# Kernel optimization log

Hardware: AMD Instinct MI355X
Metric: run time of the kernel (lower is better)

The kernel has to match this reference:

```python
import jax, jax.numpy as jnp
import numpy as np

H = 8        # num_heads
D = 64       # qkv_dim
E = 512      # embed_dim = H*D
MS = 16      # ms_hidden_dim


def setup_inputs() -> dict:
    key = jax.random.key(0)
    ks = jax.random.split(key, 12)
    b, r, c = 4, 512, 512
    row_emb = jax.random.normal(ks[0], (b, r, E), dtype=jnp.float32)
    col_emb = jax.random.normal(ks[1], (b, c, E), dtype=jnp.float32)
    cost_mat = jax.random.uniform(ks[2], (b, r, c), dtype=jnp.float32)
    attn_mask = jax.random.randint(ks[3], (b, H, r, c), 0, 2) > 0
    s = 1.0 / np.sqrt(E)
    Wq = jax.random.uniform(ks[4], (H * D, E), minval=-s, maxval=s)
    Wk = jax.random.uniform(ks[5], (H * D, E), minval=-s, maxval=s)
    Wv = jax.random.uniform(ks[6], (H * D, E), minval=-s, maxval=s)
    Wout = jax.random.uniform(ks[7], (E, E), minval=-s, maxval=s)
    m1 = np.sqrt(0.5)
    m2 = np.sqrt(1.0 / MS)
    Wmix1 = jax.random.uniform(ks[8], (H * MS, 2 * H), minval=-m1, maxval=m1)
    Wmix2 = jax.random.uniform(ks[9], (H, H * MS), minval=-m2, maxval=m2)
    return {"row_emb": row_emb, "col_emb": col_emb, "cost_mat": cost_mat,
            "attn_mask": attn_mask, "Wq": Wq, "Wk": Wk, "Wv": Wv,
            "Wmix1": Wmix1, "Wmix2": Wmix2, "Wout": Wout}


def reference(row_emb, col_emb, cost_mat, attn_mask, Wq, Wk, Wv, Wmix1, Wmix2, Wout):
    b, r, _ = row_emb.shape
    c = col_emb.shape[1]
    norm = 1.0 / jnp.sqrt(jnp.asarray(D, row_emb.dtype))
    # projections -> [b, h, s, d]
    q = (row_emb @ Wq.T).reshape(b, r, H, D).transpose(0, 2, 1, 3)
    k = (col_emb @ Wk.T).reshape(b, c, H, D).transpose(0, 2, 1, 3)
    v = (col_emb @ Wv.T).reshape(b, c, H, D).transpose(0, 2, 1, 3)
    dot = norm * jnp.einsum('bhrd,bhcd->bhrc', q, k)            # [b,h,r,c]
    cost = jnp.broadcast_to(cost_mat[:, None, :, :], dot.shape)  # [b,h,r,c]
    # stack then rearrange 'b h r c s -> b r c (h s)' (h major, s minor)
    two = jnp.stack([dot, cost], axis=-1)                        # [b,h,r,c,2]
    two = two.transpose(0, 2, 3, 1, 4).reshape(b, r, c, 2 * H)
    hid = jax.nn.relu(two @ Wmix1.T)                             # [b,r,c,H*MS]
    ms = hid @ Wmix2.T                                           # [b,r,c,H]
    logits = ms.transpose(0, 3, 1, 2)                            # [b,h,r,c]
    # mask handling: rows that are fully masked become fully unmasked
    all_masked = jnp.all(attn_mask, axis=-1, keepdims=True)
    mask = jnp.where(all_masked, False, attn_mask)
    logits = jnp.where(mask, -jnp.inf, logits)
    weights = jax.nn.softmax(logits, axis=-1)
    out = jnp.einsum('bhrc,bhcd->bhrd', weights, v)              # [b,h,r,d]
    out = out.transpose(0, 2, 1, 3).reshape(b, r, H * D)         # b s (h d)
    return out @ Wout.T
```

## Files before the change

### kernel.cpp

```cpp
#include <hip/hip_runtime.h>
#include <math.h>

typedef __attribute__((ext_vector_type(8))) short bf16x8;
typedef __attribute__((ext_vector_type(4))) float f32x4;
typedef unsigned short ushort_t;

static __device__ inline unsigned short f2bf(float f) {
    union { float f; unsigned u; } v; v.f = f;
    unsigned r = v.u + 0x7fff + ((v.u >> 16) & 1);
    return (unsigned short)(r >> 16);
}

#if defined(__has_builtin)
#  if __has_builtin(__builtin_amdgcn_cvt_pk_bf16_f32)
#    define HAVE_PK_BF16 1
#  endif
#endif

static __device__ inline unsigned pk2bf(float a, float b) {
#ifdef HAVE_PK_BF16
    auto r = __builtin_amdgcn_cvt_pk_bf16_f32(a, b);
    unsigned u; __builtin_memcpy(&u, &r, 4);
    return u;
#else
    return (unsigned)f2bf(a) | ((unsigned)f2bf(b) << 16);
#endif
}

__global__ __launch_bounds__(256) void convert_all(const float* __restrict__ a0,
                                                   const float* __restrict__ a1,
                                                   const float* __restrict__ a2,
                                                   const float* __restrict__ a3,
                                                   const float* __restrict__ a4,
                                                   const float* __restrict__ a5,
                                                   ushort_t* __restrict__ dst) {
    const size_t e = ((size_t)blockIdx.x * 256 + threadIdx.x) * 4;
    const float* src; size_t off;
    if      (e < 1048576) { src = a0; off = 0; }
    else if (e < 2097152) { src = a1; off = 1048576; }
    else if (e < 2359296) { src = a2; off = 2097152; }
    else if (e < 2621440) { src = a3; off = 2359296; }
    else if (e < 2883584) { src = a4; off = 2621440; }
    else                  { src = a5; off = 2883584; }
    const float4 v = *(const float4*)(src + (e - off));
    uint2 o; o.x = pk2bf(v.x, v.y); o.y = pk2bf(v.z, v.w);
    *(uint2*)(dst + e) = o;
}

__global__ __launch_bounds__(256) void gemm_qkv(const ushort_t* __restrict__ rowb,
                                                const ushort_t* __restrict__ colb,
                                                const ushort_t* __restrict__ Wqb,
                                                const ushort_t* __restrict__ Wkb,
                                                const ushort_t* __restrict__ Wvb,
                                                ushort_t* __restrict__ Qb,
                                                ushort_t* __restrict__ Kb,
                                                ushort_t* __restrict__ Vt) {
    const int z = blockIdx.z;
    const ushort_t* A = (z == 0) ? rowb : colb;
    const ushort_t* B = (z == 0) ? Wqb : (z == 1) ? Wkb : Wvb;

    const int t    = threadIdx.x;
    const int w    = t >> 6;
    const int lane = t & 63;
    const int quad = lane >> 4;
    const int sl   = lane & 15;
    const int m0 = blockIdx.x * 64 + (w >> 1) * 32;
    const int n0 = blockIdx.y * 64 + (w & 1) * 32;

    f32x4 acc[2][2] = {};

    for (int k0 = 0; k0 < 512; k0 += 32) {
        bf16x8 a[2], b[2];
#pragma unroll
        for (int rs = 0; rs < 2; ++rs)
            a[rs] = *(const bf16x8*)(A + (size_t)(m0 + rs * 16 + sl) * 512 + k0 + quad * 8);
#pragma unroll
        for (int cs = 0; cs < 2; ++cs)
            b[cs] = *(const bf16x8*)(B + (size_t)(n0 + cs * 16 + sl) * 512 + k0 + quad * 8);
#pragma unroll
        for (int rs = 0; rs < 2; ++rs)
#pragma unroll
            for (int cs = 0; cs < 2; ++cs)
                acc[rs][cs] = __builtin_amdgcn_mfma_f32_16x16x32_bf16(a[rs], b[cs], acc[rs][cs], 0, 0, 0);
    }

#pragma unroll
    for (int rs = 0; rs < 2; ++rs)
#pragma unroll
        for (int cs = 0; cs < 2; ++cs) {
            const int n = n0 + cs * 16 + sl;
            if (z == 2) {
                const int mb   = m0 + rs * 16 + quad * 4;
                const int bidx = mb >> 9, c = mb & 511;
                const int h = n >> 6, d = n & 63;
                ushort4 o;
                o.x = f2bf(acc[rs][cs][0]); o.y = f2bf(acc[rs][cs][1]);
                o.z = f2bf(acc[rs][cs][2]); o.w = f2bf(acc[rs][cs][3]);
                *(ushort4*)(Vt + (size_t)(((bidx * 8 + h) * 64 + d)) * 512 + c) = o;
            } else {
                ushort_t* C = (z == 0) ? Qb : Kb;
#pragma unroll
                for (int reg = 0; reg < 4; ++reg) {
                    const int m = m0 + rs * 16 + quad * 4 + reg;
                    C[(size_t)m * 512 + n] = f2bf(acc[rs][cs][reg]);
                }
            }
        }
}

__global__ __launch_bounds__(256) void gemm_out(const ushort_t* __restrict__ A,
                                                const ushort_t* __restrict__ B,
                                                float* __restrict__ C) {
    const int t    = threadIdx.x;
    const int w    = t >> 6;
    const int lane = t & 63;
    const int quad = lane >> 4;
    const int sl   = lane & 15;
    const int m0 = blockIdx.x * 64 + (w >> 1) * 32;
    const int n0 = blockIdx.y * 64 + (w & 1) * 32;

    f32x4 acc[2][2] = {};

    for (int k0 = 0; k0 < 512; k0 += 32) {
        bf16x8 a[2], b[2];
#pragma unroll
        for (int rs = 0; rs < 2; ++rs)
            a[rs] = *(const bf16x8*)(A + (size_t)(m0 + rs * 16 + sl) * 512 + k0 + quad * 8);
#pragma unroll
        for (int cs = 0; cs < 2; ++cs)
            b[cs] = *(const bf16x8*)(B + (size_t)(n0 + cs * 16 + sl) * 512 + k0 + quad * 8);
#pragma unroll
        for (int rs = 0; rs < 2; ++rs)
#pragma unroll
            for (int cs = 0; cs < 2; ++cs)
                acc[rs][cs] = __builtin_amdgcn_mfma_f32_16x16x32_bf16(a[rs], b[cs], acc[rs][cs], 0, 0, 0);
    }

#pragma unroll
    for (int rs = 0; rs < 2; ++rs)
#pragma unroll
        for (int cs = 0; cs < 2; ++cs) {
            const int n = n0 + cs * 16 + sl;
#pragma unroll
            for (int reg = 0; reg < 4; ++reg) {
                const int m = m0 + rs * 16 + quad * 4 + reg;
                C[(size_t)m * 512 + n] = acc[rs][cs][reg];
            }
        }
}

__global__ __launch_bounds__(512) void dot_mlp_v4(const ushort_t* __restrict__ Qb,
                                                  const ushort_t* __restrict__ Kb,
                                                  const float* __restrict__ cost,
                                                  const float* __restrict__ W1,
                                                  const float* __restrict__ W2,
                                                  float* __restrict__ logits) {
    __shared__ ushort_t Xs[1024 * 18];
    __shared__ ushort_t hidS[8 * 16 * 36];
    __shared__ ushort_t W1fs[128 * 16];
    __shared__ ushort_t W2ss[8 * 128];

    const int b  = blockIdx.z;
    const int r0 = blockIdx.y * 32;
    const int c0 = blockIdx.x * 32;
    const int t    = threadIdx.x;
    const int w    = t >> 6;
    const int lane = t & 63;
    const int quad = lane >> 4;
    const int sl   = lane & 15;

    const bf16x8 zf = {0, 0, 0, 0, 0, 0, 0, 0};

    if (t < 128) {
        float s = 0.f;
#pragma unroll
        for (int h = 0; h < 8; ++h) {
            W1fs[t * 16 + h] = f2bf(W1[t * 16 + 2 * h]);
            s += W1[t * 16 + 2 * h + 1];
        }
        W1fs[t * 16 + 8] = f2bf(s);
#pragma unroll
        for (int k = 9; k < 16; ++k) W1fs[t * 16 + k] = 0;
    }
#pragma unroll
    for (int i = 0; i < 2; ++i) W2ss[t + i * 512] = f2bf(W2[t + i * 512]);

#pragma unroll
    for (int i = 0; i < 2; ++i) {
        const int cell = t + i * 512;
        const int rl = cell >> 5, cl = cell & 31;
        unsigned* base = (unsigned*)(Xs + cell * 18 + 8);
        base[0] = (unsigned)f2bf(cost[((size_t)b * 512 + r0 + rl) * 512 + c0 + cl]);
        base[1] = 0; base[2] = 0; base[3] = 0; base[4] = 0;
    }

    {
        const int h = w;
        bf16x8 af[2][2], bfr[2][2];
#pragma unroll
        for (int rs = 0; rs < 2; ++rs)
#pragma unroll
            for (int ks = 0; ks < 2; ++ks)
                af[rs][ks] = *(const bf16x8*)(Qb +
                    ((size_t)(b * 512 + r0 + rs * 16 + sl) * 512 + h * 64 + ks * 32 + quad * 8));
#pragma unroll
        for (int cs = 0; cs < 2; ++cs)
#pragma unroll
            for (int ks = 0; ks < 2; ++ks)
                bfr[cs][ks] = *(const bf16x8*)(Kb +
                    ((size_t)(b * 512 + c0 + cs * 16 + sl) * 512 + h * 64 + ks * 32 + quad * 8));
#pragma unroll
        for (int rs = 0; rs < 2; ++rs)
#pragma unroll
            for (int cs = 0; cs < 2; ++cs) {
                f32x4 acc = {0.f, 0.f, 0.f, 0.f};
                acc = __builtin_amdgcn_mfma_f32_16x16x32_bf16(af[rs][0], bfr[cs][0], acc, 0, 0, 0);
                acc = __builtin_amdgcn_mfma_f32_16x16x32_bf16(af[rs][1], bfr[cs][1], acc, 0, 0, 0);
#pragma unroll
                for (int reg = 0; reg < 4; ++reg) {
                    const int cell = (rs * 16 + quad * 4 + reg) * 32 + cs * 16 + sl;
                    Xs[cell * 18 + h] = f2bf(acc[reg] * 0.125f);
                }
            }
    }

    __syncthreads();

    bf16x8 bw1[8];
#pragma unroll
    for (int nt = 0; nt < 8; ++nt)
        bw1[nt] = (quad < 2) ? *(const bf16x8*)&W1fs[(nt * 16 + sl) * 16 + quad * 8] : zf;
    bf16x8 bw2[4];
#pragma unroll
    for (int ks = 0; ks < 4; ++ks) {
        union { ushort_t s[8]; bf16x8 v; } tu;
#pragma unroll
        for (int i = 0; i < 8; ++i) {
            const int p  = quad * 8 + i;
            const int jc = (p >> 1) | ((p & 1) << 4);
            tu.s[i] = (sl < 8) ? W2ss[sl * 128 + ks * 32 + jc] : (ushort_t)0;
        }
        bw2[ks] = tu.v;
    }

    ushort_t* hidW = hidS + w * (16 * 36);

#pragma unroll
    for (int mt = 0; mt < 8; ++mt) {
        const int gmt = w * 8 + mt;
        const int cb  = gmt * 16;

        bf16x8 a1 = zf;
        if (quad < 2) {
            const unsigned* xr = (const unsigned*)Xs + (size_t)(cb + sl) * 9 + quad * 4;
            union { unsigned u[4]; bf16x8 v; } tmp;
            tmp.u[0] = xr[0]; tmp.u[1] = xr[1]; tmp.u[2] = xr[2]; tmp.u[3] = xr[3];
            a1 = tmp.v;
        }

        f32x4 acc2 = {0.f, 0.f, 0.f, 0.f};
#pragma unroll
        for (int ks = 0; ks < 4; ++ks) {
            f32x4 z = {0.f, 0.f, 0.f, 0.f};
            const f32x4 h0 = __builtin_amdgcn_mfma_f32_16x16x32_bf16(a1, bw1[2 * ks],     z, 0, 0, 0);
            const f32x4 h1 = __builtin_amdgcn_mfma_f32_16x16x32_bf16(a1, bw1[2 * ks + 1], z, 0, 0, 0);
#pragma unroll
            for (int rp = 0; rp < 4; ++rp)
                ((unsigned*)hidW)[(quad * 4 + rp) * 18 + sl] =
                    pk2bf(fmaxf(h0[rp], 0.f), fmaxf(h1[rp], 0.f));
            union { uint2 u2[2]; bf16x8 v; } tu;
            const ushort_t* hp = hidW + sl * 36 + quad * 8;
            tu.u2[0] = *(const uint2*)hp;
            tu.u2[1] = *(const uint2*)(hp + 4);
            acc2 = __builtin_amdgcn_mfma_f32_16x16x32_bf16(tu.v, bw2[ks], acc2, 0, 0, 0);
        }

        if (sl < 8) {
            const int r = r0 + (gmt >> 1);
            const int cbase = c0 + (gmt & 1) * 16 + quad * 4;
            float4 o; o.x = acc2[0]; o.y = acc2[1]; o.z = acc2[2]; o.w = acc2[3];
            *(float4*)&logits[((size_t)(b * 8 + sl) * 512 + r) * 512 + cbase] = o;
        }
    }
}

__global__ __launch_bounds__(256) void softmax_pv(const float* __restrict__ logits,
                                                  const int* __restrict__ mask,
                                                  const ushort_t* __restrict__ Vt,
                                                  ushort_t* __restrict__ Aout) {
    __shared__ ushort_t Ps[32 * 520];

    const int t    = threadIdx.x;
    const int w    = t >> 6;
    const int lane = t & 63;
    const int quad = lane >> 4;
    const int sl   = lane & 15;
    const int rt = blockIdx.x;
    const int bh = blockIdx.y;
    const int r0 = rt * 32;

#pragma unroll
    for (int rr = 0; rr < 8; ++rr) {
        const int row = w * 8 + rr;
        const float* lp = logits + ((size_t)bh * 512 + r0 + row) * 512;
        const int*   mp = mask   + ((size_t)bh * 512 + r0 + row) * 512;

        float v[8]; int m[8]; int allm = 1;
#pragma unroll
        for (int i = 0; i < 8; ++i) {
            v[i] = lp[lane + i * 64];
            m[i] = mp[lane + i * 64];
            allm &= (m[i] != 0);
        }
        const bool all_masked = (__all(allm) != 0);

        float mx = -__builtin_inff();
#pragma unroll
        for (int i = 0; i < 8; ++i) {
            const bool keep = all_masked || (m[i] == 0);
            if (keep) mx = fmaxf(mx, v[i]);
        }
#pragma unroll
        for (int s = 32; s > 0; s >>= 1) mx = fmaxf(mx, __shfl_xor(mx, s, 64));

        float e[8]; float sum = 0.f;
#pragma unroll
        for (int i = 0; i < 8; ++i) {
            const bool keep = all_masked || (m[i] == 0);
            e[i] = keep ? __expf(v[i] - mx) : 0.f;
            sum += e[i];
        }
#pragma unroll
        for (int s = 32; s > 0; s >>= 1) sum += __shfl_xor(sum, s, 64);

        const float inv = 1.f / sum;
#pragma unroll
        for (int i = 0; i < 8; ++i)
            Ps[row * 520 + lane + i * 64] = f2bf(e[i] * inv);
    }

    __syncthreads();

    const int mt  = w >> 1;
    const int n0w = (w & 1) * 32;
    const ushort_t* vb = Vt + (size_t)bh * 64 * 512;

    f32x4 acc[2] = {};
    for (int ks = 0; ks < 16; ++ks) {
        union { uint2 u2[2]; bf16x8 v; } ta;
        const ushort_t* pp = Ps + (size_t)(mt * 16 + sl) * 520 + ks * 32 + quad * 8;
        ta.u2[0] = *(const uint2*)pp;
        ta.u2[1] = *(const uint2*)(pp + 4);
        bf16x8 bv[2];
#pragma unroll
        for (int cn = 0; cn < 2; ++cn)
            bv[cn] = *(const bf16x8*)(vb + (size_t)(n0w + cn * 16 + sl) * 512 + ks * 32 + quad * 8);
#pragma unroll
        for (int cn = 0; cn < 2; ++cn)
            acc[cn] = __builtin_amdgcn_mfma_f32_16x16x32_bf16(ta.v, bv[cn], acc[cn], 0, 0, 0);
    }

    const int bidx = bh >> 3, h = bh & 7;
    ushort_t* Cb = Aout + (size_t)bidx * 512 * 512 + h * 64;
#pragma unroll
    for (int cn = 0; cn < 2; ++cn) {
        const int n = n0w + cn * 16 + sl;
#pragma unroll
        for (int reg = 0; reg < 4; ++reg) {
            const int m = r0 + mt * 16 + quad * 4 + reg;
            Cb[(size_t)m * 512 + n] = f2bf(acc[cn][reg]);
        }
    }
}

extern "C" void kernel_launch(void* const* d_in, const int* in_sizes, int n_in,
                              void* d_out, int out_size, void* d_ws, size_t ws_size,
                              hipStream_t stream) {
    const float* row_emb = (const float*)d_in[0];
    const float* col_emb = (const float*)d_in[1];
    const float* cost    = (const float*)d_in[2];
    const int*   mask    = (const int*)d_in[3];
    const float* Wq      = (const float*)d_in[4];
    const float* Wk      = (const float*)d_in[5];
    const float* Wv      = (const float*)d_in[6];
    const float* Wmix1   = (const float*)d_in[7];
    const float* Wmix2   = (const float*)d_in[8];
    const float* Wout    = (const float*)d_in[9];
    float* out = (float*)d_out;

    char* ws = (char*)d_ws;
    const size_t MB = (size_t)1 << 20;
    ushort_t* convDst = (ushort_t*)ws;
    ushort_t* rowb  = (ushort_t*)(ws);
    ushort_t* colb  = (ushort_t*)(ws + 2 * MB);
    ushort_t* Wqb   = (ushort_t*)(ws + 4 * MB);
    ushort_t* Wkb   = (ushort_t*)(ws + 4 * MB + 512 * 1024);
    ushort_t* Wvb   = (ushort_t*)(ws + 5 * MB);
    ushort_t* Woutb = (ushort_t*)(ws + 5 * MB + 512 * 1024);
    ushort_t* Qb    = (ushort_t*)(ws + 6 * MB);
    ushort_t* Kb    = (ushort_t*)(ws + 8 * MB);
    ushort_t* Vt    = (ushort_t*)(ws + 10 * MB);
    ushort_t* Aoutb = (ushort_t*)(ws + 12 * MB);
    float* logitsBuf = (float*)(ws + 40 * MB);

    convert_all<<<3072, 256, 0, stream>>>(row_emb, col_emb, Wq, Wk, Wv, Wout, convDst);

    gemm_qkv<<<dim3(32, 8, 3), 256, 0, stream>>>(rowb, colb, Wqb, Wkb, Wvb, Qb, Kb, Vt);

    dot_mlp_v4<<<dim3(16, 16, 4), 512, 0, stream>>>(Qb, Kb, cost, Wmix1, Wmix2, logitsBuf);

    softmax_pv<<<dim3(16, 32), 256, 0, stream>>>(logitsBuf, mask, Vt, Aoutb);

    gemm_out<<<dim3(32, 8), 256, 0, stream>>>(Aoutb, Woutb, out);
}
```

Measured before the change: 185.6 us.

## Transpose MLP MFMAs to keep hidden activations in registers, drop LDS staging

The mixing MLP is recomputed transposed (weights as the A operand, features as B), so the first MFMA's output layout matches the B-operand layout the second MFMA needs. Hidden activations are converted to bf16 in registers, which removes the per-warp shared-memory round trip and the hidS buffer. In exchange each lane holds eight accumulator tiles, raising register pressure. Logit stores become per-head scalar stores (16 contiguous columns per head) instead of float4 stores, which may coalesce less well.

```diff
diff --git a/kernel.cpp b/kernel.cpp
--- a/kernel.cpp
+++ b/kernel.cpp
@@ -149,14 +149,13 @@
         }
 }
 
-__global__ __launch_bounds__(512) void dot_mlp_v4(const ushort_t* __restrict__ Qb,
+__global__ __launch_bounds__(512) void dot_mlp_v5(const ushort_t* __restrict__ Qb,
                                                   const ushort_t* __restrict__ Kb,
                                                   const float* __restrict__ cost,
                                                   const float* __restrict__ W1,
                                                   const float* __restrict__ W2,
                                                   float* __restrict__ logits) {
     __shared__ ushort_t Xs[1024 * 18];
-    __shared__ ushort_t hidS[8 * 16 * 36];
     __shared__ ushort_t W1fs[128 * 16];
     __shared__ ushort_t W2ss[8 * 128];
 
@@ -226,24 +225,22 @@
 
     __syncthreads();
 
-    bf16x8 bw1[8];
+    bf16x8 aw1[8];
 #pragma unroll
     for (int nt = 0; nt < 8; ++nt)
-        bw1[nt] = (quad < 2) ? *(const bf16x8*)&W1fs[(nt * 16 + sl) * 16 + quad * 8] : zf;
-    bf16x8 bw2[4];
+        aw1[nt] = (quad < 2) ? *(const bf16x8*)&W1fs[(nt * 16 + sl) * 16 + quad * 8] : zf;
+
+    bf16x8 w2f[4];
 #pragma unroll
     for (int ks = 0; ks < 4; ++ks) {
         union { ushort_t s[8]; bf16x8 v; } tu;
 #pragma unroll
         for (int i = 0; i < 8; ++i) {
-            const int p  = quad * 8 + i;
-            const int jc = (p >> 1) | ((p & 1) << 4);
-            tu.s[i] = (sl < 8) ? W2ss[sl * 128 + ks * 32 + jc] : (ushort_t)0;
-        }
-        bw2[ks] = tu.v;
-    }
-
-    ushort_t* hidW = hidS + w * (16 * 36);
+            const int j = (2 * ks + (i >> 2)) * 16 + quad * 4 + (i & 3);
+            tu.s[i] = (sl < 8) ? W2ss[sl * 128 + j] : (ushort_t)0;
+        }
+        w2f[ks] = tu.v;
+    }
 
 #pragma unroll
     for (int mt = 0; mt < 8; ++mt) {
@@ -258,28 +255,32 @@
             a1 = tmp.v;
         }
 
+        f32x4 hT[8];
+#pragma unroll
+        for (int j = 0; j < 8; ++j) {
+            f32x4 z = {0.f, 0.f, 0.f, 0.f};
+            hT[j] = __builtin_amdgcn_mfma_f32_16x16x32_bf16(aw1[j], a1, z, 0, 0, 0);
+        }
+
         f32x4 acc2 = {0.f, 0.f, 0.f, 0.f};
 #pragma unroll
         for (int ks = 0; ks < 4; ++ks) {
-            f32x4 z = {0.f, 0.f, 0.f, 0.f};
-            const f32x4 h0 = __builtin_amdgcn_mfma_f32_16x16x32_bf16(a1, bw1[2 * ks],     z, 0, 0, 0);
-            const f32x4 h1 = __builtin_amdgcn_mfma_f32_16x16x32_bf16(a1, bw1[2 * ks + 1], z, 0, 0, 0);
-#pragma unroll
-            for (int rp = 0; rp < 4; ++rp)
-                ((unsigned*)hidW)[(quad * 4 + rp) * 18 + sl] =
-                    pk2bf(fmaxf(h0[rp], 0.f), fmaxf(h1[rp], 0.f));
-            union { uint2 u2[2]; bf16x8 v; } tu;
-            const ushort_t* hp = hidW + sl * 36 + quad * 8;
-            tu.u2[0] = *(const uint2*)hp;
-            tu.u2[1] = *(const uint2*)(hp + 4);
-            acc2 = __builtin_amdgcn_mfma_f32_16x16x32_bf16(tu.v, bw2[ks], acc2, 0, 0, 0);
-        }
-
-        if (sl < 8) {
+            union { unsigned u[4]; bf16x8 v; } hb;
+            hb.u[0] = pk2bf(fmaxf(hT[2 * ks][0], 0.f),     fmaxf(hT[2 * ks][1], 0.f));
+            hb.u[1] = pk2bf(fmaxf(hT[2 * ks][2], 0.f),     fmaxf(hT[2 * ks][3], 0.f));
+            hb.u[2] = pk2bf(fmaxf(hT[2 * ks + 1][0], 0.f), fmaxf(hT[2 * ks + 1][1], 0.f));
+            hb.u[3] = pk2bf(fmaxf(hT[2 * ks + 1][2], 0.f), fmaxf(hT[2 * ks + 1][3], 0.f));
+            acc2 = __builtin_amdgcn_mfma_f32_16x16x32_bf16(w2f[ks], hb.v, acc2, 0, 0, 0);
+        }
+
+        if (quad < 2) {
             const int r = r0 + (gmt >> 1);
-            const int cbase = c0 + (gmt & 1) * 16 + quad * 4;
-            float4 o; o.x = acc2[0]; o.y = acc2[1]; o.z = acc2[2]; o.w = acc2[3];
-            *(float4*)&logits[((size_t)(b * 8 + sl) * 512 + r) * 512 + cbase] = o;
+            const int c = c0 + (gmt & 1) * 16 + sl;
+#pragma unroll
+            for (int reg = 0; reg < 4; ++reg) {
+                const int h = quad * 4 + reg;
+                logits[((size_t)(b * 8 + h) * 512 + r) * 512 + c] = acc2[reg];
+            }
         }
     }
 }
@@ -407,7 +408,7 @@
 
     gemm_qkv<<<dim3(32, 8, 3), 256, 0, stream>>>(rowb, colb, Wqb, Wkb, Wvb, Qb, Kb, Vt);
 
-    dot_mlp_v4<<<dim3(16, 16, 4), 512, 0, stream>>>(Qb, Kb, cost, Wmix1, Wmix2, logitsBuf);
+    dot_mlp_v5<<<dim3(16, 16, 4), 512, 0, stream>>>(Qb, Kb, cost, Wmix1, Wmix2, logitsBuf);
 
     softmax_pv<<<dim3(16, 32), 256, 0, stream>>>(logitsBuf, mask, Vt, Aoutb);
 
```

Result: no change. 183.7 us (-1.0%).
